# Kernel optimization log

Measured on AMD Instinct MI355X. Metric: run time of the kernel, lower is better.

## Reference

```python
import jax, jax.numpy as jnp
import numpy as np

H, DH = 8, 16  # num_heads, head_dim (out_feats // num_heads)
NP, NA, NS = 100000, 60000, 1000


def _gat_conv(feat_src, feat_dst, n_dst, src, dst, W, al, ar, b):
    # DGL GATConv (eval mode: feat_drop/attn_drop are identity)
    hs = (feat_src @ W).reshape(-1, H, DH)          # [Ns,H,D]
    hd = (feat_dst @ W).reshape(-1, H, DH)          # [Nd,H,D]
    el = (hs * al).sum(-1)                          # [Ns,H]
    er = (hd * ar).sum(-1)                          # [Nd,H]
    e = jax.nn.leaky_relu(el[src] + er[dst], negative_slope=0.2)  # [E,H]
    # segment softmax over edges sharing a destination node
    emax = jax.ops.segment_max(e, dst, num_segments=n_dst)
    emax = jnp.where(jnp.isfinite(emax), emax, 0.0)
    ee = jnp.exp(e - emax[dst])
    denom = jax.ops.segment_sum(ee, dst, num_segments=n_dst)
    alpha = ee / jnp.maximum(denom[dst], 1e-9)      # [E,H]
    m = jax.ops.segment_sum(alpha[:, :, None] * hs[src], dst, num_segments=n_dst)
    return m.reshape(n_dst, H * DH) + b             # [Nd, out_feats]


def setup_inputs() -> dict:
    key = jax.random.key(0)
    ks = jax.random.split(key, 18)
    Epa, Eps = 300000, 150000
    f32 = jnp.float32
    inp = {
        "feat_paper_0": jax.random.normal(ks[0], (NP, 128), f32),
        "feat_author_0": jax.random.normal(ks[1], (NA, 128), f32),
        "feat_subject_0": jax.random.normal(ks[2], (NS, 128), f32),
        "feat_paper_1": jax.random.normal(ks[3], (NP, 128), f32),
        "feat_author_1": jax.random.normal(ks[4], (NA, 128), f32),
        "feat_subject_1": jax.random.normal(ks[5], (NS, 128), f32),
        "pa_src": jax.random.randint(ks[6], (Epa,), 0, NP, jnp.int32),
        "pa_dst": jax.random.randint(ks[7], (Epa,), 0, NA, jnp.int32),
        "ap_src": jax.random.randint(ks[8], (Epa,), 0, NA, jnp.int32),
        "ap_dst": jax.random.randint(ks[9], (Epa,), 0, NP, jnp.int32),
        "ps_src": jax.random.randint(ks[10], (Eps,), 0, NP, jnp.int32),
        "ps_dst": jax.random.randint(ks[11], (Eps,), 0, NS, jnp.int32),
        "sp_src": jax.random.randint(ks[12], (Eps,), 0, NS, jnp.int32),
        "sp_dst": jax.random.randint(ks[13], (Eps,), 0, NP, jnp.int32),
        "Ws": jax.random.normal(ks[14], (4, 128, 128), f32) * 0.08,
        "als": jax.random.normal(ks[15], (4, H, DH), f32) * 0.1,
        "ars": jax.random.normal(ks[16], (4, H, DH), f32) * 0.1,
        "bs": jnp.zeros((4, 128), f32),
    }
    return inp


def reference(feat_paper_0, feat_author_0, feat_subject_0,
              feat_paper_1, feat_author_1, feat_subject_1,
              pa_src, pa_dst, ap_src, ap_dst, ps_src, ps_dst, sp_src, sp_dst,
              Ws, als, ars, bs):
    def one_input(fp, fa, fs):
        # rel 0: paper->author, 1: author->paper, 2: paper->subject, 3: subject->paper
        h_author = _gat_conv(fp, fa, NA, pa_src, pa_dst, Ws[0], als[0], ars[0], bs[0])
        h_paper_ap = _gat_conv(fa, fp, NP, ap_src, ap_dst, Ws[1], als[1], ars[1], bs[1])
        h_subject = _gat_conv(fp, fs, NS, ps_src, ps_dst, Ws[2], als[2], ars[2], bs[2])
        h_paper_sp = _gat_conv(fs, fp, NP, sp_src, sp_dst, Ws[3], als[3], ars[3], bs[3])
        h_paper = (h_paper_ap + h_paper_sp) * 0.5  # HeteroGraphConv aggregate='mean'
        # act = identity; key order for ACM: [paper, author, subject]
        return jnp.concatenate([h_paper, h_author, h_subject], axis=0)

    out0 = one_input(feat_paper_0, feat_author_0, feat_subject_0)
    out1 = one_input(feat_paper_1, feat_author_1, feat_subject_1)
    return jnp.stack([out0, out1], axis=0)  # [2, NP+NA+NS, 128]
```

## Files before the change

kernel.cpp:

```cpp
#include <hip/hip_runtime.h>

#define NHEAD 8
#define NPAPER 100000
#define NAUTHOR 60000
#define NSUBJ 1000
#define NTOT (NPAPER + NAUTHOR + NSUBJ)
#define NDEG 261000

typedef __attribute__((ext_vector_type(8))) short bf16x8;
typedef __attribute__((ext_vector_type(4))) float f32x4;

__device__ __forceinline__ unsigned short f2bf(float x) {
    unsigned int u = __builtin_bit_cast(unsigned int, x);
    u += 0x7fffu + ((u >> 16) & 1u);
    return (unsigned short)(u >> 16);
}
__device__ __forceinline__ float bf2f_lo(unsigned int v) {
    return __builtin_bit_cast(float, v << 16);
}
__device__ __forceinline__ float bf2f_hi(unsigned int v) {
    return __builtin_bit_cast(float, v & 0xffff0000u);
}

__global__ void prep_kernel(const float* __restrict__ Ws, const float* __restrict__ als,
                            const float* __restrict__ ars,
                            unsigned short* __restrict__ Wt,
                            unsigned short* __restrict__ combo) {
    int idx = blockIdx.x * 256 + threadIdx.x;
    if (idx < 65536) {
        int r = idx >> 14, rem = idx & 16383, c = rem >> 7, k = rem & 127;
        Wt[idx] = f2bf(Ws[(r << 14) + k * 128 + c]);
    } else if (idx < 65536 + 8192) {
        int j = idx - 65536;
        int r = j >> 11, rem = j & 2047, n = rem >> 7, k = rem & 127;
        int p = r ^ 1;
        const float *W, *a;
        if (n < 8) {
            W = Ws + (r << 14) + k * 128 + n * 16;
            a = als + r * 128 + n * 16;
        } else {
            int h = n - 8;
            W = Ws + (p << 14) + k * 128 + h * 16;
            a = ars + p * 128 + h * 16;
        }
        float s = 0.f;
#pragma unroll
        for (int d = 0; d < 16; ++d) s += W[d] * a[d];
        combo[j] = f2bf(s);
    }
}

struct CsrPtrs {
    const int* esrc[4];
    const int* edst[4];
    int ebase[5];
    int nbase[4];
};

__global__ void csr_count(CsrPtrs cp, int* __restrict__ deg) {
    int idx = blockIdx.x * 256 + threadIdx.x;
    if (idx >= cp.ebase[4]) return;
    int r = 0;
    while (idx >= cp.ebase[r + 1]) ++r;
    int e = idx - cp.ebase[r];
    atomicAdd(&deg[cp.nbase[r] + cp.edst[r][e]], 1);
}

__global__ void csr_scatter(CsrPtrs cp, int* __restrict__ cursor,
                            int* __restrict__ srcs) {
    int idx = blockIdx.x * 256 + threadIdx.x;
    if (idx >= cp.ebase[4]) return;
    int r = 0;
    while (idx >= cp.ebase[r + 1]) ++r;
    int e = idx - cp.ebase[r];
    int p = atomicAdd(&cursor[cp.nbase[r] + cp.edst[r][e]], 1);
    srcs[p] = cp.esrc[r][e];
}

__global__ __launch_bounds__(256) void scan_bsum(const int* __restrict__ deg,
                                                 int* __restrict__ bsums, int N) {
    int base = blockIdx.x * 1024 + threadIdx.x * 4;
    int s = 0;
#pragma unroll
    for (int j = 0; j < 4; ++j) {
        int i = base + j;
        if (i < N) s += deg[i];
    }
#pragma unroll
    for (int off = 32; off; off >>= 1) s += __shfl_down(s, off);
    __shared__ int wt[4];
    if ((threadIdx.x & 63) == 0) wt[threadIdx.x >> 6] = s;
    __syncthreads();
    if (threadIdx.x == 0) bsums[blockIdx.x] = wt[0] + wt[1] + wt[2] + wt[3];
}

__global__ __launch_bounds__(256) void scan_small_excl(int* __restrict__ data, int n) {
    int t = threadIdx.x;
    int v = (t < n) ? data[t] : 0;
    int inc = v;
#pragma unroll
    for (int off = 1; off < 64; off <<= 1) {
        int u = __shfl_up(inc, off);
        if ((t & 63) >= off) inc += u;
    }
    __shared__ int wt[4];
    if ((t & 63) == 63) wt[t >> 6] = inc;
    __syncthreads();
    int wo = 0;
    for (int w = 0; w < (t >> 6); ++w) wo += wt[w];
    if (t < n) data[t] = wo + inc - v;
}

__global__ __launch_bounds__(256) void scan_final(const int* __restrict__ deg,
                                                  const int* __restrict__ bsums,
                                                  int* __restrict__ row_ptr,
                                                  int* __restrict__ cursor, int N) {
    int t = threadIdx.x;
    int base = blockIdx.x * 1024 + t * 4;
    int d[4];
    int s = 0;
#pragma unroll
    for (int j = 0; j < 4; ++j) {
        int i = base + j;
        d[j] = (i < N) ? deg[i] : 0;
        s += d[j];
    }
    int inc = s;
#pragma unroll
    for (int off = 1; off < 64; off <<= 1) {
        int u = __shfl_up(inc, off);
        if ((t & 63) >= off) inc += u;
    }
    __shared__ int wt[4];
    if ((t & 63) == 63) wt[t >> 6] = inc;
    __syncthreads();
    int start = bsums[blockIdx.x];
    for (int w = 0; w < (t >> 6); ++w) start += wt[w];
    start += inc - s;
#pragma unroll
    for (int j = 0; j < 4; ++j) {
        int i = base + j;
        if (i < N) {
            row_ptr[i] = start;
            cursor[i] = start;
        }
        start += d[j];
    }
    if (base < N && base + 4 >= N) row_ptr[N] = start;
}

struct ProjArgs {
    const float* A[8];
    const unsigned short* Wt[8];
    const unsigned short* cb[8];
    unsigned short* hs[8];
    float* el[8];
    float* er[8];
    int N[8];
    int blk0[9];
};

__global__ __launch_bounds__(256) void project_kernel(ProjArgs args) {
    int bb = blockIdx.x;
    int t = 0;
    while (bb >= args.blk0[t + 1]) ++t;
    const float* A = args.A[t];
    const unsigned short* Wt = args.Wt[t];
    const unsigned short* cb = args.cb[t];
    unsigned short* hs = args.hs[t];
    float* el = args.el[t];
    float* er = args.er[t];
    const int N = args.N[t];
    const int row0 = (bb - args.blk0[t]) * 64;

    __shared__ unsigned short Abf[64 * 128];
    __shared__ unsigned short Wl[144 * 128];
    const int tid = threadIdx.x;

#pragma unroll
    for (int it = 0; it < 4; ++it) {
        int id = it * 256 + tid;
        int r = id >> 4, c8 = id & 15;
        int row = row0 + r;
        if (row >= N) row = N - 1;
        const float4* ap = reinterpret_cast<const float4*>(A + (size_t)row * 128 + c8 * 8);
        float4 v0 = ap[0], v1 = ap[1];
        uint4 pk;
        pk.x = (unsigned)f2bf(v0.x) | ((unsigned)f2bf(v0.y) << 16);
        pk.y = (unsigned)f2bf(v0.z) | ((unsigned)f2bf(v0.w) << 16);
        pk.z = (unsigned)f2bf(v1.x) | ((unsigned)f2bf(v1.y) << 16);
        pk.w = (unsigned)f2bf(v1.z) | ((unsigned)f2bf(v1.w) << 16);
        *reinterpret_cast<uint4*>(&Abf[(r * 16 + (c8 ^ (r & 15))) * 8]) = pk;
    }
#pragma unroll
    for (int it = 0; it < 9; ++it) {
        int id = it * 256 + tid;
        int r = id >> 4, c8 = id & 15;
        const unsigned short* srcp = (r < 128) ? (Wt + r * 128) : (cb + (r - 128) * 128);
        uint4 v = *reinterpret_cast<const uint4*>(srcp + c8 * 8);
        *reinterpret_cast<uint4*>(&Wl[(r * 16 + (c8 ^ (r & 15))) * 8]) = v;
    }
    __syncthreads();

    const int l = tid & 63;
    const int w = tid >> 6;
    const int lrow = l & 15;
    const int lk8 = l >> 4;

    bf16x8 af[4];
    const int arow = w * 16 + lrow;
#pragma unroll
    for (int ks = 0; ks < 4; ++ks) {
        int c8 = ks * 4 + lk8;
        af[ks] = *reinterpret_cast<const bf16x8*>(
            &Abf[(arow * 16 + (c8 ^ (arow & 15))) * 8]);
    }
    __syncthreads();

#pragma unroll
    for (int t9 = 0; t9 < 9; ++t9) {
        f32x4 acc = f32x4{0.f, 0.f, 0.f, 0.f};
#pragma unroll
        for (int ks = 0; ks < 4; ++ks) {
            int wrow = t9 * 16 + lrow;
            int c8 = ks * 4 + lk8;
            bf16x8 bf = *reinterpret_cast<const bf16x8*>(
                &Wl[(wrow * 16 + (c8 ^ (wrow & 15))) * 8]);
            acc = __builtin_amdgcn_mfma_f32_16x16x32_bf16(af[ks], bf, acc, 0, 0, 0);
        }
        if (t9 < 8) {
#pragma unroll
            for (int r = 0; r < 4; ++r) {
                int rl = w * 16 + lk8 * 4 + r;
                int col = t9 * 16 + lrow;
                Abf[(rl * 16 + ((col >> 3) ^ (rl & 15))) * 8 + (col & 7)] = f2bf(acc[r]);
            }
        } else {
#pragma unroll
            for (int r = 0; r < 4; ++r) {
                int row = row0 + w * 16 + lk8 * 4 + r;
                if (row < N) {
                    if (lrow < 8) el[(size_t)row * 8 + lrow] = acc[r];
                    else er[(size_t)row * 8 + (lrow - 8)] = acc[r];
                }
            }
        }
    }
    __syncthreads();

#pragma unroll
    for (int it = 0; it < 4; ++it) {
        int id = it * 256 + tid;
        int r = id >> 4, c8 = id & 15;
        int row = row0 + r;
        if (row < N) {
            uint4 v = *reinterpret_cast<const uint4*>(&Abf[(r * 16 + (c8 ^ (r & 15))) * 8]);
            *reinterpret_cast<uint4*>(hs + (size_t)row * 128 + c8 * 8) = v;
        }
    }
}

__device__ __forceinline__ void acc_list(int p0, int p1, float erd, int l, int h,
                                         const int* __restrict__ srcs,
                                         const float* __restrict__ el,
                                         const unsigned short* __restrict__ hs,
                                         float* A, float& DS) {
    float a4[4][8];
    float dv[4] = {0.f, 0.f, 0.f, 0.f};
#pragma unroll
    for (int u = 0; u < 4; ++u)
#pragma unroll
        for (int j = 0; j < 8; ++j) a4[u][j] = 0.f;
    int p = p0;
    for (; p + 4 <= p1; p += 4) {
        int sx[4];
#pragma unroll
        for (int u = 0; u < 4; ++u) sx[u] = srcs[p + u];
        float ev[4];
        uint4 q[4];
#pragma unroll
        for (int u = 0; u < 4; ++u) {
            ev[u] = el[(size_t)sx[u] * 8 + h] + erd;
            q[u] = *reinterpret_cast<const uint4*>(hs + (size_t)sx[u] * 128 + l * 8);
        }
#pragma unroll
        for (int u = 0; u < 4; ++u) {
            float e = ev[u];
            e = e > 0.f ? e : 0.2f * e;
            float ee = __expf(e);
            dv[u] += ee;
            a4[u][0] += ee * bf2f_lo(q[u].x);
            a4[u][1] += ee * bf2f_hi(q[u].x);
            a4[u][2] += ee * bf2f_lo(q[u].y);
            a4[u][3] += ee * bf2f_hi(q[u].y);
            a4[u][4] += ee * bf2f_lo(q[u].z);
            a4[u][5] += ee * bf2f_hi(q[u].z);
            a4[u][6] += ee * bf2f_lo(q[u].w);
            a4[u][7] += ee * bf2f_hi(q[u].w);
        }
    }
    for (; p < p1; ++p) {
        int s = srcs[p];
        float e = el[(size_t)s * 8 + h] + erd;
        e = e > 0.f ? e : 0.2f * e;
        float ee = __expf(e);
        uint4 q = *reinterpret_cast<const uint4*>(hs + (size_t)s * 128 + l * 8);
        dv[0] += ee;
        a4[0][0] += ee * bf2f_lo(q.x);
        a4[0][1] += ee * bf2f_hi(q.x);
        a4[0][2] += ee * bf2f_lo(q.y);
        a4[0][3] += ee * bf2f_hi(q.y);
        a4[0][4] += ee * bf2f_lo(q.z);
        a4[0][5] += ee * bf2f_hi(q.z);
        a4[0][6] += ee * bf2f_lo(q.w);
        a4[0][7] += ee * bf2f_hi(q.w);
    }
#pragma unroll
    for (int j = 0; j < 8; ++j) A[j] = a4[0][j] + a4[1][j] + a4[2][j] + a4[3][j];
    DS = dv[0] + dv[1] + dv[2] + dv[3];
}

__global__ __launch_bounds__(256) void agg_author(
    const int* __restrict__ rp, const int* __restrict__ srcs,
    const float* __restrict__ el0, const float* __restrict__ el1,
    const float* __restrict__ er0, const float* __restrict__ er1,
    const unsigned short* __restrict__ hs0, const unsigned short* __restrict__ hs1,
    const float* __restrict__ b, float* __restrict__ out0, float* __restrict__ out1) {
    int g = (blockIdx.x * 256 + threadIdx.x) >> 4;
    int l = threadIdx.x & 15;
    if (g >= 2 * NAUTHOR) return;
    int inp = g >= NAUTHOR;
    int dst = inp ? g - NAUTHOR : g;
    const float* el = inp ? el1 : el0;
    const float* er = inp ? er1 : er0;
    const unsigned short* hs = inp ? hs1 : hs0;
    float* out = inp ? out1 : out0;
    int h = l >> 1;
    int p0 = rp[dst], p1 = rp[dst + 1];
    float erd = er[(size_t)dst * 8 + h];
    float A[8], ds;
    acc_list(p0, p1, erd, l, h, srcs, el, hs, A, ds);
    float inv = 1.f / fmaxf(ds, 1e-9f);
    const float4* bp = reinterpret_cast<const float4*>(b + l * 8);
    float4 b0 = bp[0], b1 = bp[1];
    float4 o0 = make_float4(A[0] * inv + b0.x, A[1] * inv + b0.y,
                            A[2] * inv + b0.z, A[3] * inv + b0.w);
    float4 o1 = make_float4(A[4] * inv + b1.x, A[5] * inv + b1.y,
                            A[6] * inv + b1.z, A[7] * inv + b1.w);
    float* op = out + (size_t)dst * 128 + l * 8;
    reinterpret_cast<float4*>(op)[0] = o0;
    reinterpret_cast<float4*>(op)[1] = o1;
}

__global__ __launch_bounds__(256) void agg_paper(
    const int* __restrict__ rp, const int* __restrict__ srcs,
    const float* __restrict__ el1a, const float* __restrict__ el1b,
    const float* __restrict__ er1a, const float* __restrict__ er1b,
    const unsigned short* __restrict__ hs1a, const unsigned short* __restrict__ hs1b,
    const float* __restrict__ el3a, const float* __restrict__ el3b,
    const float* __restrict__ er3a, const float* __restrict__ er3b,
    const unsigned short* __restrict__ hs3a, const unsigned short* __restrict__ hs3b,
    const float* __restrict__ b1, const float* __restrict__ b3,
    float* __restrict__ out0, float* __restrict__ out1) {
    int g = (blockIdx.x * 256 + threadIdx.x) >> 4;
    int l = threadIdx.x & 15;
    if (g >= 2 * NPAPER) return;
    int inp = g >= NPAPER;
    int dst = inp ? g - NPAPER : g;
    const float* el1 = inp ? el1b : el1a;
    const float* er1 = inp ? er1b : er1a;
    const unsigned short* hs1 = inp ? hs1b : hs1a;
    const float* el3 = inp ? el3b : el3a;
    const float* er3 = inp ? er3b : er3a;
    const unsigned short* hs3 = inp ? hs3b : hs3a;
    float* out = inp ? out1 : out0;
    int h = l >> 1;

    float A1[8], A3[8], d1, d3;
    {
        int p0 = rp[60000 + dst], p1 = rp[60000 + dst + 1];
        acc_list(p0, p1, er1[(size_t)dst * 8 + h], l, h, srcs, el1, hs1, A1, d1);
    }
    {
        int p0 = rp[161000 + dst], p1 = rp[161000 + dst + 1];
        acc_list(p0, p1, er3[(size_t)dst * 8 + h], l, h, srcs, el3, hs3, A3, d3);
    }
    float i1 = 1.f / fmaxf(d1, 1e-9f);
    float i3 = 1.f / fmaxf(d3, 1e-9f);
    const float4* bp1 = reinterpret_cast<const float4*>(b1 + l * 8);
    const float4* bp3 = reinterpret_cast<const float4*>(b3 + l * 8);
    float4 b10 = bp1[0], b11 = bp1[1], b30 = bp3[0], b31 = bp3[1];
    float4 o0, o1;
    o0.x = 0.5f * ((A1[0] * i1 + b10.x) + (A3[0] * i3 + b30.x));
    o0.y = 0.5f * ((A1[1] * i1 + b10.y) + (A3[1] * i3 + b30.y));
    o0.z = 0.5f * ((A1[2] * i1 + b10.z) + (A3[2] * i3 + b30.z));
    o0.w = 0.5f * ((A1[3] * i1 + b10.w) + (A3[3] * i3 + b30.w));
    o1.x = 0.5f * ((A1[4] * i1 + b11.x) + (A3[4] * i3 + b31.x));
    o1.y = 0.5f * ((A1[5] * i1 + b11.y) + (A3[5] * i3 + b31.y));
    o1.z = 0.5f * ((A1[6] * i1 + b11.z) + (A3[6] * i3 + b31.z));
    o1.w = 0.5f * ((A1[7] * i1 + b11.w) + (A3[7] * i3 + b31.w));
    float* op = out + (size_t)dst * 128 + l * 8;
    reinterpret_cast<float4*>(op)[0] = o0;
    reinterpret_cast<float4*>(op)[1] = o1;
}

__global__ __launch_bounds__(256) void agg_subject(
    const int* __restrict__ rp, const int* __restrict__ srcs,
    const float* __restrict__ el0, const float* __restrict__ el1,
    const float* __restrict__ er0, const float* __restrict__ er1,
    const unsigned short* __restrict__ hs0, const unsigned short* __restrict__ hs1,
    const float* __restrict__ b, float* __restrict__ out0, float* __restrict__ out1) {
    int blk = blockIdx.x;
    int inp = blk >= NSUBJ;
    int dst = inp ? blk - NSUBJ : blk;
    const float* el = inp ? el1 : el0;
    const float* er = inp ? er1 : er0;
    const unsigned short* hs = inp ? hs1 : hs0;
    float* out = inp ? out1 : out0;
    int gl = threadIdx.x >> 4;
    int l = threadIdx.x & 15;
    int h = l >> 1;
    int p0 = rp[160000 + dst], p1 = rp[160000 + dst + 1];
    float erd = er[(size_t)dst * 8 + h];
    float a[8];
#pragma unroll
    for (int j = 0; j < 8; ++j) a[j] = 0.f;
    float dsum = 0.f;
    for (int p = p0 + gl; p < p1; p += 16) {
        int s = srcs[p];
        float e = el[(size_t)s * 8 + h] + erd;
        e = e > 0.f ? e : 0.2f * e;
        float ee = __expf(e);
        uint4 q = *reinterpret_cast<const uint4*>(hs + (size_t)s * 128 + l * 8);
        dsum += ee;
        a[0] += ee * bf2f_lo(q.x);
        a[1] += ee * bf2f_hi(q.x);
        a[2] += ee * bf2f_lo(q.y);
        a[3] += ee * bf2f_hi(q.y);
        a[4] += ee * bf2f_lo(q.z);
        a[5] += ee * bf2f_hi(q.z);
        a[6] += ee * bf2f_lo(q.w);
        a[7] += ee * bf2f_hi(q.w);
    }
    __shared__ float Am[16][128];
    __shared__ float Dm[16][8];
#pragma unroll
    for (int j = 0; j < 8; ++j) Am[gl][l * 8 + j] = a[j];
    if ((l & 1) == 0) Dm[gl][h] = dsum;
    __syncthreads();
    int c = threadIdx.x;
    if (c < 128) {
        float s = 0.f, dn = 0.f;
        int hh = c >> 4;
#pragma unroll
        for (int g = 0; g < 16; ++g) {
            s += Am[g][c];
            dn += Dm[g][hh];
        }
        out[(size_t)dst * 128 + c] = s / fmaxf(dn, 1e-9f) + b[c];
    }
}

extern "C" void kernel_launch(void* const* d_in, const int* in_sizes, int n_in,
                              void* d_out, int out_size, void* d_ws, size_t ws_size,
                              hipStream_t stream) {
    const float* Ws4 = (const float*)d_in[14];
    const float* als = (const float*)d_in[15];
    const float* ars = (const float*)d_in[16];
    const float* bs = (const float*)d_in[17];
    float* out = (float*)d_out;

    const int Es[4] = {in_sizes[6], in_sizes[8], in_sizes[10], in_sizes[12]};
    const int Nsrcs[4] = {NPAPER, NAUTHOR, NPAPER, NSUBJ};
    const int Ndsts[4] = {NAUTHOR, NPAPER, NSUBJ, NPAPER};
    const int Etot = Es[0] + Es[1] + Es[2] + Es[3];

    char* wsp = (char*)d_ws;
    auto carve = [&](size_t bytes) {
        char* p = wsp;
        wsp += (bytes + 255) & ~(size_t)255;
        return p;
    };
    unsigned short* Wt = (unsigned short*)carve(4 * 16384 * 2);
    unsigned short* combo = (unsigned short*)carve(4 * 2048 * 2);
    unsigned short* hsb[2][4];
    float* elb[2][4];
    float* erb[2][4];
    for (int i = 0; i < 2; ++i)
        for (int r = 0; r < 4; ++r) {
            hsb[i][r] = (unsigned short*)carve((size_t)Nsrcs[r] * 128 * 2);
            elb[i][r] = (float*)carve((size_t)Nsrcs[r] * 8 * 4);
            erb[i][r] = (float*)carve((size_t)Ndsts[r] * 8 * 4);
        }
    int* deg = (int*)carve((size_t)NDEG * 4);
    int* cursor = (int*)carve((size_t)NDEG * 4);
    int* bsums = (int*)carve(1024);
    int* rp = (int*)carve((size_t)(NDEG + 1) * 4);
    int* scsr = (int*)carve((size_t)Etot * 4);

    CsrPtrs cp;
    cp.esrc[0] = (const int*)d_in[6];  cp.edst[0] = (const int*)d_in[7];
    cp.esrc[1] = (const int*)d_in[8];  cp.edst[1] = (const int*)d_in[9];
    cp.esrc[2] = (const int*)d_in[10]; cp.edst[2] = (const int*)d_in[11];
    cp.esrc[3] = (const int*)d_in[12]; cp.edst[3] = (const int*)d_in[13];
    cp.ebase[0] = 0;
    for (int r = 0; r < 4; ++r) cp.ebase[r + 1] = cp.ebase[r] + Es[r];
    cp.nbase[0] = 0;
    cp.nbase[1] = 60000;
    cp.nbase[2] = 160000;
    cp.nbase[3] = 161000;

    prep_kernel<<<288, 256, 0, stream>>>(Ws4, als, ars, Wt, combo);
    hipMemsetAsync(deg, 0, (size_t)NDEG * 4, stream);
    csr_count<<<(Etot + 255) / 256, 256, 0, stream>>>(cp, deg);
    int nb = (NDEG + 1023) / 1024;
    scan_bsum<<<nb, 256, 0, stream>>>(deg, bsums, NDEG);
    scan_small_excl<<<1, 256, 0, stream>>>(bsums, nb);
    scan_final<<<nb, 256, 0, stream>>>(deg, bsums, rp, cursor, NDEG);
    csr_scatter<<<(Etot + 255) / 256, 256, 0, stream>>>(cp, cursor, scsr);

    ProjArgs pa;
    int blk = 0;
    int ti = 0;
    for (int i = 0; i < 2; ++i) {
        const float* feats[3] = {(const float*)d_in[0 + 3 * i],
                                 (const float*)d_in[1 + 3 * i],
                                 (const float*)d_in[2 + 3 * i]};
        const int srcT[4] = {0, 2, 1, 3};
        for (int k = 0; k < 4; ++k) {
            int r = srcT[k];
            const int featT[4] = {0, 1, 0, 2};
            const float* A = feats[featT[r]];
            int N = Nsrcs[r];
            pa.A[ti] = A;
            pa.Wt[ti] = Wt + (size_t)r * 16384;
            pa.cb[ti] = combo + (size_t)r * 2048;
            pa.hs[ti] = hsb[i][r];
            pa.el[ti] = elb[i][r];
            pa.er[ti] = erb[i][r ^ 1];
            pa.N[ti] = N;
            pa.blk0[ti] = blk;
            blk += (N + 63) / 64;
            ++ti;
        }
    }
    pa.blk0[8] = blk;
    project_kernel<<<blk, 256, 0, stream>>>(pa);

    float* out0 = out;
    float* out1 = out + (size_t)NTOT * 128;

    agg_author<<<(2 * NAUTHOR * 16 + 255) / 256, 256, 0, stream>>>(
        rp, scsr, elb[0][0], elb[1][0], erb[0][0], erb[1][0], hsb[0][0], hsb[1][0],
        bs + 0, out0 + (size_t)NPAPER * 128, out1 + (size_t)NPAPER * 128);
    agg_paper<<<(2 * NPAPER * 16 + 255) / 256, 256, 0, stream>>>(
        rp, scsr,
        elb[0][1], elb[1][1], erb[0][1], erb[1][1], hsb[0][1], hsb[1][1],
        elb[0][3], elb[1][3], erb[0][3], erb[1][3], hsb[0][3], hsb[1][3],
        bs + 128, bs + 384, out0, out1);
    agg_subject<<<2 * NSUBJ, 256, 0, stream>>>(
        rp, scsr, elb[0][2], elb[1][2], erb[0][2], erb[1][2], hsb[0][2], hsb[1][2],
        bs + 256, out0 + (size_t)(NPAPER + NAUTHOR) * 128,
        out1 + (size_t)(NPAPER + NAUTHOR) * 128);
}
```

Baseline: 402.8 us.

## Fuse launches: memset into prep, count into projection, single aggregation kernel

```diff
diff --git a/kernel.cpp b/kernel.cpp
--- a/kernel.cpp
+++ b/kernel.cpp
@@ -25,8 +25,14 @@
 __global__ void prep_kernel(const float* __restrict__ Ws, const float* __restrict__ als,
                             const float* __restrict__ ars,
                             unsigned short* __restrict__ Wt,
-                            unsigned short* __restrict__ combo) {
-    int idx = blockIdx.x * 256 + threadIdx.x;
+                            unsigned short* __restrict__ combo, int* __restrict__ deg) {
+    int b = blockIdx.x;
+    if (b >= 288) {
+        int idx = (b - 288) * 1024 + threadIdx.x * 4;
+        if (idx < NDEG) *reinterpret_cast<int4*>(&deg[idx]) = int4{0, 0, 0, 0};
+        return;
+    }
+    int idx = b * 256 + threadIdx.x;
     if (idx < 65536) {
         int r = idx >> 14, rem = idx & 16383, c = rem >> 7, k = rem & 127;
         Wt[idx] = f2bf(Ws[(r << 14) + k * 128 + c]);
@@ -50,132 +56,110 @@
     }
 }
 
-struct CsrPtrs {
-    const int* esrc[4];
+__device__ __forceinline__ void stage_W(unsigned short* Wl, const unsigned short* Wt,
+                                        const unsigned short* cb, int tid) {
+#pragma unroll
+    for (int it = 0; it < 9; ++it) {
+        int id = it * 256 + tid;
+        int r = id >> 4, c8 = id & 15;
+        const unsigned short* srcp = (r < 128) ? (Wt + r * 128) : (cb + (r - 128) * 128);
+        uint4 v = *reinterpret_cast<const uint4*>(srcp + c8 * 8);
+        *reinterpret_cast<uint4*>(&Wl[(r * 16 + (c8 ^ (r & 15))) * 8]) = v;
+    }
+}
+
+__device__ __forceinline__ void mfma_set(const unsigned short* Wl, unsigned short* Abf,
+                                         const bf16x8* af, int tid, int row0, int N,
+                                         float* __restrict__ el, float* __restrict__ er) {
+    const int l = tid & 63, w = tid >> 6, lrow = l & 15, lk8 = l >> 4;
+#pragma unroll
+    for (int t9 = 0; t9 < 9; ++t9) {
+        f32x4 acc = f32x4{0.f, 0.f, 0.f, 0.f};
+#pragma unroll
+        for (int ks = 0; ks < 4; ++ks) {
+            int wrow = t9 * 16 + lrow;
+            int c8 = ks * 4 + lk8;
+            bf16x8 bf = *reinterpret_cast<const bf16x8*>(
+                &Wl[(wrow * 16 + (c8 ^ (wrow & 15))) * 8]);
+            acc = __builtin_amdgcn_mfma_f32_16x16x32_bf16(af[ks], bf, acc, 0, 0, 0);
+        }
+        if (t9 < 8) {
+#pragma unroll
+            for (int r = 0; r < 4; ++r) {
+                int rl = w * 16 + lk8 * 4 + r;
+                int col = t9 * 16 + lrow;
+                Abf[(rl * 16 + ((col >> 3) ^ (rl & 15))) * 8 + (col & 7)] = f2bf(acc[r]);
+            }
+        } else {
+#pragma unroll
+            for (int r = 0; r < 4; ++r) {
+                int row = row0 + w * 16 + lk8 * 4 + r;
+                if (row < N) {
+                    if (lrow < 8) el[(size_t)row * 8 + lrow] = acc[r];
+                    else er[(size_t)row * 8 + (lrow - 8)] = acc[r];
+                }
+            }
+        }
+    }
+}
+
+__device__ __forceinline__ void store_hs(const unsigned short* Abf,
+                                         unsigned short* __restrict__ hs, int tid,
+                                         int row0, int N) {
+#pragma unroll
+    for (int it = 0; it < 4; ++it) {
+        int id = it * 256 + tid;
+        int r = id >> 4, c8 = id & 15;
+        int row = row0 + r;
+        if (row < N) {
+            uint4 v = *reinterpret_cast<const uint4*>(&Abf[(r * 16 + (c8 ^ (r & 15))) * 8]);
+            *reinterpret_cast<uint4*>(hs + (size_t)row * 128 + c8 * 8) = v;
+        }
+    }
+}
+
+struct PCArgs {
     const int* edst[4];
     int ebase[5];
     int nbase[4];
+    int* deg;
+    int cblk;
+    const float* A[6];
+    int N[6];
+    int blk0[7];
+    const unsigned short* Wt1[6];
+    const unsigned short* cb1[6];
+    unsigned short* hs1[6];
+    float* el1[6];
+    float* er1[6];
+    const unsigned short* Wt2[6];
+    const unsigned short* cb2[6];
+    unsigned short* hs2[6];
+    float* el2[6];
+    float* er2[6];
+    int has2[6];
 };
 
-__global__ void csr_count(CsrPtrs cp, int* __restrict__ deg) {
-    int idx = blockIdx.x * 256 + threadIdx.x;
-    if (idx >= cp.ebase[4]) return;
-    int r = 0;
-    while (idx >= cp.ebase[r + 1]) ++r;
-    int e = idx - cp.ebase[r];
-    atomicAdd(&deg[cp.nbase[r] + cp.edst[r][e]], 1);
-}
-
-__global__ void csr_scatter(CsrPtrs cp, int* __restrict__ cursor,
-                            int* __restrict__ srcs) {
-    int idx = blockIdx.x * 256 + threadIdx.x;
-    if (idx >= cp.ebase[4]) return;
-    int r = 0;
-    while (idx >= cp.ebase[r + 1]) ++r;
-    int e = idx - cp.ebase[r];
-    int p = atomicAdd(&cursor[cp.nbase[r] + cp.edst[r][e]], 1);
-    srcs[p] = cp.esrc[r][e];
-}
-
-__global__ __launch_bounds__(256) void scan_bsum(const int* __restrict__ deg,
-                                                 int* __restrict__ bsums, int N) {
-    int base = blockIdx.x * 1024 + threadIdx.x * 4;
-    int s = 0;
-#pragma unroll
-    for (int j = 0; j < 4; ++j) {
-        int i = base + j;
-        if (i < N) s += deg[i];
-    }
-#pragma unroll
-    for (int off = 32; off; off >>= 1) s += __shfl_down(s, off);
-    __shared__ int wt[4];
-    if ((threadIdx.x & 63) == 0) wt[threadIdx.x >> 6] = s;
-    __syncthreads();
-    if (threadIdx.x == 0) bsums[blockIdx.x] = wt[0] + wt[1] + wt[2] + wt[3];
-}
-
-__global__ __launch_bounds__(256) void scan_small_excl(int* __restrict__ data, int n) {
-    int t = threadIdx.x;
-    int v = (t < n) ? data[t] : 0;
-    int inc = v;
-#pragma unroll
-    for (int off = 1; off < 64; off <<= 1) {
-        int u = __shfl_up(inc, off);
-        if ((t & 63) >= off) inc += u;
-    }
-    __shared__ int wt[4];
-    if ((t & 63) == 63) wt[t >> 6] = inc;
-    __syncthreads();
-    int wo = 0;
-    for (int w = 0; w < (t >> 6); ++w) wo += wt[w];
-    if (t < n) data[t] = wo + inc - v;
-}
-
-__global__ __launch_bounds__(256) void scan_final(const int* __restrict__ deg,
-                                                  const int* __restrict__ bsums,
-                                                  int* __restrict__ row_ptr,
-                                                  int* __restrict__ cursor, int N) {
-    int t = threadIdx.x;
-    int base = blockIdx.x * 1024 + t * 4;
-    int d[4];
-    int s = 0;
-#pragma unroll
-    for (int j = 0; j < 4; ++j) {
-        int i = base + j;
-        d[j] = (i < N) ? deg[i] : 0;
-        s += d[j];
-    }
-    int inc = s;
-#pragma unroll
-    for (int off = 1; off < 64; off <<= 1) {
-        int u = __shfl_up(inc, off);
-        if ((t & 63) >= off) inc += u;
-    }
-    __shared__ int wt[4];
-    if ((t & 63) == 63) wt[t >> 6] = inc;
-    __syncthreads();
-    int start = bsums[blockIdx.x];
-    for (int w = 0; w < (t >> 6); ++w) start += wt[w];
-    start += inc - s;
-#pragma unroll
-    for (int j = 0; j < 4; ++j) {
-        int i = base + j;
-        if (i < N) {
-            row_ptr[i] = start;
-            cursor[i] = start;
-        }
-        start += d[j];
-    }
-    if (base < N && base + 4 >= N) row_ptr[N] = start;
-}
-
-struct ProjArgs {
-    const float* A[8];
-    const unsigned short* Wt[8];
-    const unsigned short* cb[8];
-    unsigned short* hs[8];
-    float* el[8];
-    float* er[8];
-    int N[8];
-    int blk0[9];
-};
-
-__global__ __launch_bounds__(256) void project_kernel(ProjArgs args) {
-    int bb = blockIdx.x;
-    int t = 0;
-    while (bb >= args.blk0[t + 1]) ++t;
-    const float* A = args.A[t];
-    const unsigned short* Wt = args.Wt[t];
-    const unsigned short* cb = args.cb[t];
-    unsigned short* hs = args.hs[t];
-    float* el = args.el[t];
-    float* er = args.er[t];
-    const int N = args.N[t];
-    const int row0 = (bb - args.blk0[t]) * 64;
-
+__global__ __launch_bounds__(256) void project_count(PCArgs a) {
     __shared__ unsigned short Abf[64 * 128];
     __shared__ unsigned short Wl[144 * 128];
+    int bb = blockIdx.x;
     const int tid = threadIdx.x;
+    if (bb < a.cblk) {
+        int idx = bb * 256 + tid;
+        if (idx < a.ebase[4]) {
+            int r = 0;
+            while (idx >= a.ebase[r + 1]) ++r;
+            atomicAdd(&a.deg[a.nbase[r] + a.edst[r][idx - a.ebase[r]]], 1);
+        }
+        return;
+    }
+    bb -= a.cblk;
+    int t = 0;
+    while (bb >= a.blk0[t + 1]) ++t;
+    const int row0 = (bb - a.blk0[t]) * 64;
+    const int N = a.N[t];
+    const float* A = a.A[t];
 
 #pragma unroll
     for (int it = 0; it < 4; ++it) {
@@ -192,21 +176,10 @@
         pk.w = (unsigned)f2bf(v1.z) | ((unsigned)f2bf(v1.w) << 16);
         *reinterpret_cast<uint4*>(&Abf[(r * 16 + (c8 ^ (r & 15))) * 8]) = pk;
     }
-#pragma unroll
-    for (int it = 0; it < 9; ++it) {
-        int id = it * 256 + tid;
-        int r = id >> 4, c8 = id & 15;
-        const unsigned short* srcp = (r < 128) ? (Wt + r * 128) : (cb + (r - 128) * 128);
-        uint4 v = *reinterpret_cast<const uint4*>(srcp + c8 * 8);
-        *reinterpret_cast<uint4*>(&Wl[(r * 16 + (c8 ^ (r & 15))) * 8]) = v;
-    }
-    __syncthreads();
-
-    const int l = tid & 63;
-    const int w = tid >> 6;
-    const int lrow = l & 15;
-    const int lk8 = l >> 4;
-
+    stage_W(Wl, a.Wt1[t], a.cb1[t], tid);
+    __syncthreads();
+
+    const int l = tid & 63, w = tid >> 6, lrow = l & 15, lk8 = l >> 4;
     bf16x8 af[4];
     const int arow = w * 16 + lrow;
 #pragma unroll
@@ -217,47 +190,100 @@
     }
     __syncthreads();
 
-#pragma unroll
-    for (int t9 = 0; t9 < 9; ++t9) {
-        f32x4 acc = f32x4{0.f, 0.f, 0.f, 0.f};
-#pragma unroll
-        for (int ks = 0; ks < 4; ++ks) {
-            int wrow = t9 * 16 + lrow;
-            int c8 = ks * 4 + lk8;
-            bf16x8 bf = *reinterpret_cast<const bf16x8*>(
-                &Wl[(wrow * 16 + (c8 ^ (wrow & 15))) * 8]);
-            acc = __builtin_amdgcn_mfma_f32_16x16x32_bf16(af[ks], bf, acc, 0, 0, 0);
-        }
-        if (t9 < 8) {
-#pragma unroll
-            for (int r = 0; r < 4; ++r) {
-                int rl = w * 16 + lk8 * 4 + r;
-                int col = t9 * 16 + lrow;
-                Abf[(rl * 16 + ((col >> 3) ^ (rl & 15))) * 8 + (col & 7)] = f2bf(acc[r]);
-            }
-        } else {
-#pragma unroll
-            for (int r = 0; r < 4; ++r) {
-                int row = row0 + w * 16 + lk8 * 4 + r;
-                if (row < N) {
-                    if (lrow < 8) el[(size_t)row * 8 + lrow] = acc[r];
-                    else er[(size_t)row * 8 + (lrow - 8)] = acc[r];
-                }
-            }
-        }
-    }
-    __syncthreads();
-
-#pragma unroll
-    for (int it = 0; it < 4; ++it) {
-        int id = it * 256 + tid;
-        int r = id >> 4, c8 = id & 15;
-        int row = row0 + r;
-        if (row < N) {
-            uint4 v = *reinterpret_cast<const uint4*>(&Abf[(r * 16 + (c8 ^ (r & 15))) * 8]);
-            *reinterpret_cast<uint4*>(hs + (size_t)row * 128 + c8 * 8) = v;
-        }
-    }
+    mfma_set(Wl, Abf, af, tid, row0, N, a.el1[t], a.er1[t]);
+    __syncthreads();
+    store_hs(Abf, a.hs1[t], tid, row0, N);
+    if (!a.has2[t]) return;
+    stage_W(Wl, a.Wt2[t], a.cb2[t], tid);
+    __syncthreads();
+    mfma_set(Wl, Abf, af, tid, row0, N, a.el2[t], a.er2[t]);
+    __syncthreads();
+    store_hs(Abf, a.hs2[t], tid, row0, N);
+}
+
+__global__ __launch_bounds__(256) void scan_bsum(const int* __restrict__ deg,
+                                                 int* __restrict__ bsums, int N) {
+    int base = blockIdx.x * 1024 + threadIdx.x * 4;
+    int s = 0;
+#pragma unroll
+    for (int j = 0; j < 4; ++j) {
+        int i = base + j;
+        if (i < N) s += deg[i];
+    }
+#pragma unroll
+    for (int off = 32; off; off >>= 1) s += __shfl_down(s, off);
+    __shared__ int wt[4];
+    if ((threadIdx.x & 63) == 0) wt[threadIdx.x >> 6] = s;
+    __syncthreads();
+    if (threadIdx.x == 0) bsums[blockIdx.x] = wt[0] + wt[1] + wt[2] + wt[3];
+}
+
+__global__ __launch_bounds__(256) void scan_final(const int* __restrict__ deg,
+                                                  const int* __restrict__ bsums,
+                                                  int* __restrict__ row_ptr,
+                                                  int* __restrict__ cursor, int N) {
+    int t = threadIdx.x;
+    __shared__ int s_start;
+    __shared__ int wsum[4];
+    {
+        int acc = 0;
+        for (int i = t; i < (int)blockIdx.x; i += 256) acc += bsums[i];
+#pragma unroll
+        for (int off = 32; off; off >>= 1) acc += __shfl_down(acc, off);
+        if ((t & 63) == 0) wsum[t >> 6] = acc;
+        __syncthreads();
+        if (t == 0) s_start = wsum[0] + wsum[1] + wsum[2] + wsum[3];
+        __syncthreads();
+    }
+    int base = blockIdx.x * 1024 + t * 4;
+    int d[4];
+    int s = 0;
+#pragma unroll
+    for (int j = 0; j < 4; ++j) {
+        int i = base + j;
+        d[j] = (i < N) ? deg[i] : 0;
+        s += d[j];
+    }
+    int inc = s;
+#pragma unroll
+    for (int off = 1; off < 64; off <<= 1) {
+        int u = __shfl_up(inc, off);
+        if ((t & 63) >= off) inc += u;
+    }
+    __shared__ int wt[4];
+    if ((t & 63) == 63) wt[t >> 6] = inc;
+    __syncthreads();
+    int start = s_start;
+    for (int w = 0; w < (t >> 6); ++w) start += wt[w];
+    start += inc - s;
+#pragma unroll
+    for (int j = 0; j < 4; ++j) {
+        int i = base + j;
+        if (i < N) {
+            row_ptr[i] = start;
+            cursor[i] = start;
+        }
+        start += d[j];
+    }
+    if (base < N && base + 4 >= N) row_ptr[N] = start;
+}
+
+struct CsrPtrs {
+    const int* esrc[4];
+    const int* edst[4];
+    int ebase[5];
+    int nbase[4];
+};
+
+__global__ void csr_scatter(CsrPtrs cp, int* __restrict__ cursor,
+                            int* __restrict__ srcs) {
+    int idx = blockIdx.x * 256 + threadIdx.x;
+    if (idx >= cp.ebase[4]) return;
+    int r = 0;
+    while (idx >= cp.ebase[r + 1]) ++r;
+    int e = idx - cp.ebase[r];
+    int p = atomicAdd(&cursor[cp.nbase[r] + cp.edst[r][e]], 1);
+    srcs[p] = cp.esrc[r][e];
 }
 
 __device__ __forceinline__ void acc_list(int p0, int p1, float erd, int l, int h,
@@ -320,144 +346,120 @@
     DS = dv[0] + dv[1] + dv[2] + dv[3];
 }
 
-__global__ __launch_bounds__(256) void agg_author(
-    const int* __restrict__ rp, const int* __restrict__ srcs,
-    const float* __restrict__ el0, const float* __restrict__ el1,
-    const float* __restrict__ er0, const float* __restrict__ er1,
-    const unsigned short* __restrict__ hs0, const unsigned short* __restrict__ hs1,
-    const float* __restrict__ b, float* __restrict__ out0, float* __restrict__ out1) {
-    int g = (blockIdx.x * 256 + threadIdx.x) >> 4;
-    int l = threadIdx.x & 15;
-    if (g >= 2 * NAUTHOR) return;
-    int inp = g >= NAUTHOR;
-    int dst = inp ? g - NAUTHOR : g;
-    const float* el = inp ? el1 : el0;
-    const float* er = inp ? er1 : er0;
-    const unsigned short* hs = inp ? hs1 : hs0;
-    float* out = inp ? out1 : out0;
-    int h = l >> 1;
-    int p0 = rp[dst], p1 = rp[dst + 1];
-    float erd = er[(size_t)dst * 8 + h];
-    float A[8], ds;
-    acc_list(p0, p1, erd, l, h, srcs, el, hs, A, ds);
-    float inv = 1.f / fmaxf(ds, 1e-9f);
-    const float4* bp = reinterpret_cast<const float4*>(b + l * 8);
-    float4 b0 = bp[0], b1 = bp[1];
-    float4 o0 = make_float4(A[0] * inv + b0.x, A[1] * inv + b0.y,
-                            A[2] * inv + b0.z, A[3] * inv + b0.w);
-    float4 o1 = make_float4(A[4] * inv + b1.x, A[5] * inv + b1.y,
-                            A[6] * inv + b1.z, A[7] * inv + b1.w);
-    float* op = out + (size_t)dst * 128 + l * 8;
-    reinterpret_cast<float4*>(op)[0] = o0;
-    reinterpret_cast<float4*>(op)[1] = o1;
-}
-
-__global__ __launch_bounds__(256) void agg_paper(
-    const int* __restrict__ rp, const int* __restrict__ srcs,
-    const float* __restrict__ el1a, const float* __restrict__ el1b,
-    const float* __restrict__ er1a, const float* __restrict__ er1b,
-    const unsigned short* __restrict__ hs1a, const unsigned short* __restrict__ hs1b,
-    const float* __restrict__ el3a, const float* __restrict__ el3b,
-    const float* __restrict__ er3a, const float* __restrict__ er3b,
-    const unsigned short* __restrict__ hs3a, const unsigned short* __restrict__ hs3b,
-    const float* __restrict__ b1, const float* __restrict__ b3,
-    float* __restrict__ out0, float* __restrict__ out1) {
-    int g = (blockIdx.x * 256 + threadIdx.x) >> 4;
-    int l = threadIdx.x & 15;
-    if (g >= 2 * NPAPER) return;
-    int inp = g >= NPAPER;
-    int dst = inp ? g - NPAPER : g;
-    const float* el1 = inp ? el1b : el1a;
-    const float* er1 = inp ? er1b : er1a;
-    const unsigned short* hs1 = inp ? hs1b : hs1a;
-    const float* el3 = inp ? el3b : el3a;
-    const float* er3 = inp ? er3b : er3a;
-    const unsigned short* hs3 = inp ? hs3b : hs3a;
-    float* out = inp ? out1 : out0;
-    int h = l >> 1;
-
-    float A1[8], A3[8], d1, d3;
-    {
-        int p0 = rp[60000 + dst], p1 = rp[60000 + dst + 1];
-        acc_list(p0, p1, er1[(size_t)dst * 8 + h], l, h, srcs, el1, hs1, A1, d1);
-    }
-    {
-        int p0 = rp[161000 + dst], p1 = rp[161000 + dst + 1];
-        acc_list(p0, p1, er3[(size_t)dst * 8 + h], l, h, srcs, el3, hs3, A3, d3);
-    }
-    float i1 = 1.f / fmaxf(d1, 1e-9f);
-    float i3 = 1.f / fmaxf(d3, 1e-9f);
-    const float4* bp1 = reinterpret_cast<const float4*>(b1 + l * 8);
-    const float4* bp3 = reinterpret_cast<const float4*>(b3 + l * 8);
-    float4 b10 = bp1[0], b11 = bp1[1], b30 = bp3[0], b31 = bp3[1];
-    float4 o0, o1;
-    o0.x = 0.5f * ((A1[0] * i1 + b10.x) + (A3[0] * i3 + b30.x));
-    o0.y = 0.5f * ((A1[1] * i1 + b10.y) + (A3[1] * i3 + b30.y));
-    o0.z = 0.5f * ((A1[2] * i1 + b10.z) + (A3[2] * i3 + b30.z));
-    o0.w = 0.5f * ((A1[3] * i1 + b10.w) + (A3[3] * i3 + b30.w));
-    o1.x = 0.5f * ((A1[4] * i1 + b11.x) + (A3[4] * i3 + b31.x));
-    o1.y = 0.5f * ((A1[5] * i1 + b11.y) + (A3[5] * i3 + b31.y));
-    o1.z = 0.5f * ((A1[6] * i1 + b11.z) + (A3[6] * i3 + b31.z));
-    o1.w = 0.5f * ((A1[7] * i1 + b11.w) + (A3[7] * i3 + b31.w));
-    float* op = out + (size_t)dst * 128 + l * 8;
-    reinterpret_cast<float4*>(op)[0] = o0;
-    reinterpret_cast<float4*>(op)[1] = o1;
-}
-
-__global__ __launch_bounds__(256) void agg_subject(
-    const int* __restrict__ rp, const int* __restrict__ srcs,
-    const float* __restrict__ el0, const float* __restrict__ el1,
-    const float* __restrict__ er0, const float* __restrict__ er1,
-    const unsigned short* __restrict__ hs0, const unsigned short* __restrict__ hs1,
-    const float* __restrict__ b, float* __restrict__ out0, float* __restrict__ out1) {
+#define PB 12500
+#define AB 7500
+#define SB 2000
+
+struct AggArgs {
+    const int* rp;
+    const int* srcs;
+    const float* el[8];
+    const float* er[8];
+    const unsigned short* hs[8];
+    const float* bs;
+    float* out0;
+    float* out1;
+};
+
+__global__ __launch_bounds__(256) void mega_agg(AggArgs a) {
     int blk = blockIdx.x;
-    int inp = blk >= NSUBJ;
-    int dst = inp ? blk - NSUBJ : blk;
-    const float* el = inp ? el1 : el0;
-    const float* er = inp ? er1 : er0;
-    const unsigned short* hs = inp ? hs1 : hs0;
-    float* out = inp ? out1 : out0;
-    int gl = threadIdx.x >> 4;
-    int l = threadIdx.x & 15;
-    int h = l >> 1;
-    int p0 = rp[160000 + dst], p1 = rp[160000 + dst + 1];
-    float erd = er[(size_t)dst * 8 + h];
-    float a[8];
-#pragma unroll
-    for (int j = 0; j < 8; ++j) a[j] = 0.f;
-    float dsum = 0.f;
-    for (int p = p0 + gl; p < p1; p += 16) {
-        int s = srcs[p];
-        float e = el[(size_t)s * 8 + h] + erd;
-        e = e > 0.f ? e : 0.2f * e;
-        float ee = __expf(e);
-        uint4 q = *reinterpret_cast<const uint4*>(hs + (size_t)s * 128 + l * 8);
-        dsum += ee;
-        a[0] += ee * bf2f_lo(q.x);
-        a[1] += ee * bf2f_hi(q.x);
-        a[2] += ee * bf2f_lo(q.y);
-        a[3] += ee * bf2f_hi(q.y);
-        a[4] += ee * bf2f_lo(q.z);
-        a[5] += ee * bf2f_hi(q.z);
-        a[6] += ee * bf2f_lo(q.w);
-        a[7] += ee * bf2f_hi(q.w);
-    }
     __shared__ float Am[16][128];
     __shared__ float Dm[16][8];
-#pragma unroll
-    for (int j = 0; j < 8; ++j) Am[gl][l * 8 + j] = a[j];
-    if ((l & 1) == 0) Dm[gl][h] = dsum;
-    __syncthreads();
-    int c = threadIdx.x;
-    if (c < 128) {
-        float s = 0.f, dn = 0.f;
-        int hh = c >> 4;
-#pragma unroll
-        for (int g = 0; g < 16; ++g) {
-            s += Am[g][c];
-            dn += Dm[g][hh];
-        }
-        out[(size_t)dst * 128 + c] = s / fmaxf(dn, 1e-9f) + b[c];
+
+    if (blk < PB) {
+        int g = blk * 16 + (threadIdx.x >> 4);
+        int l = threadIdx.x & 15, h = l >> 1;
+        int inp = g >= NPAPER;
+        int dst = inp ? g - NPAPER : g;
+        float* out = (inp ? a.out1 : a.out0) + (size_t)dst * 128 + l * 8;
+        float A1[8], A3[8], d1, d3;
+        acc_list(a.rp[60000 + dst], a.rp[60000 + dst + 1],
+                 a.er[inp * 4 + 1][(size_t)dst * 8 + h], l, h, a.srcs,
+                 a.el[inp * 4 + 1], a.hs[inp * 4 + 1], A1, d1);
+        acc_list(a.rp[161000 + dst], a.rp[161000 + dst + 1],
+                 a.er[inp * 4 + 3][(size_t)dst * 8 + h], l, h, a.srcs,
+                 a.el[inp * 4 + 3], a.hs[inp * 4 + 3], A3, d3);
+        float i1 = 1.f / fmaxf(d1, 1e-9f);
+        float i3 = 1.f / fmaxf(d3, 1e-9f);
+        const float4* bp1 = reinterpret_cast<const float4*>(a.bs + 128 + l * 8);
+        const float4* bp3 = reinterpret_cast<const float4*>(a.bs + 384 + l * 8);
+        float4 b10 = bp1[0], b11 = bp1[1], b30 = bp3[0], b31 = bp3[1];
+        float4 o0, o1;
+        o0.x = 0.5f * ((A1[0] * i1 + b10.x) + (A3[0] * i3 + b30.x));
+        o0.y = 0.5f * ((A1[1] * i1 + b10.y) + (A3[1] * i3 + b30.y));
+        o0.z = 0.5f * ((A1[2] * i1 + b10.z) + (A3[2] * i3 + b30.z));
+        o0.w = 0.5f * ((A1[3] * i1 + b10.w) + (A3[3] * i3 + b30.w));
+        o1.x = 0.5f * ((A1[4] * i1 + b11.x) + (A3[4] * i3 + b31.x));
+        o1.y = 0.5f * ((A1[5] * i1 + b11.y) + (A3[5] * i3 + b31.y));
+        o1.z = 0.5f * ((A1[6] * i1 + b11.z) + (A3[6] * i3 + b31.z));
+        o1.w = 0.5f * ((A1[7] * i1 + b11.w) + (A3[7] * i3 + b31.w));
+        reinterpret_cast<float4*>(out)[0] = o0;
+        reinterpret_cast<float4*>(out)[1] = o1;
+    } else if (blk < PB + AB) {
+        int g = (blk - PB) * 16 + (threadIdx.x >> 4);
+        int l = threadIdx.x & 15, h = l >> 1;
+        int inp = g >= NAUTHOR;
+        int dst = inp ? g - NAUTHOR : g;
+        float* out = (inp ? a.out1 : a.out0) + (size_t)(NPAPER + dst) * 128 + l * 8;
+        float A[8], ds;
+        acc_list(a.rp[dst], a.rp[dst + 1], a.er[inp * 4 + 0][(size_t)dst * 8 + h], l, h,
+                 a.srcs, a.el[inp * 4 + 0], a.hs[inp * 4 + 0], A, ds);
+        float inv = 1.f / fmaxf(ds, 1e-9f);
+        const float4* bp = reinterpret_cast<const float4*>(a.bs + l * 8);
+        float4 b0 = bp[0], b1 = bp[1];
+        float4 o0 = make_float4(A[0] * inv + b0.x, A[1] * inv + b0.y,
+                                A[2] * inv + b0.z, A[3] * inv + b0.w);
+        float4 o1 = make_float4(A[4] * inv + b1.x, A[5] * inv + b1.y,
+                                A[6] * inv + b1.z, A[7] * inv + b1.w);
+        reinterpret_cast<float4*>(out)[0] = o0;
+        reinterpret_cast<float4*>(out)[1] = o1;
+    } else {
+        int b2 = blk - (PB + AB);
+        int inp = b2 >= NSUBJ;
+        int dst = inp ? b2 - NSUBJ : b2;
+        const float* el = a.el[inp * 4 + 2];
+        const float* er = a.er[inp * 4 + 2];
+        const unsigned short* hs = a.hs[inp * 4 + 2];
+        float* out = (inp ? a.out1 : a.out0) + (size_t)(NPAPER + NAUTHOR + dst) * 128;
+        int gl = threadIdx.x >> 4;
+        int l = threadIdx.x & 15, h = l >> 1;
+        int p0 = a.rp[160000 + dst], p1 = a.rp[160000 + dst + 1];
+        float erd = er[(size_t)dst * 8 + h];
+        float acc8[8];
+#pragma unroll
+        for (int j = 0; j < 8; ++j) acc8[j] = 0.f;
+        float dsum = 0.f;
+        for (int p = p0 + gl; p < p1; p += 16) {
+            int s = a.srcs[p];
+            float e = el[(size_t)s * 8 + h] + erd;
+            e = e > 0.f ? e : 0.2f * e;
+            float ee = __expf(e);
+            uint4 q = *reinterpret_cast<const uint4*>(hs + (size_t)s * 128 + l * 8);
+            dsum += ee;
+            acc8[0] += ee * bf2f_lo(q.x);
+            acc8[1] += ee * bf2f_hi(q.x);
+            acc8[2] += ee * bf2f_lo(q.y);
+            acc8[3] += ee * bf2f_hi(q.y);
+            acc8[4] += ee * bf2f_lo(q.z);
+            acc8[5] += ee * bf2f_hi(q.z);
+            acc8[6] += ee * bf2f_lo(q.w);
+            acc8[7] += ee * bf2f_hi(q.w);
+        }
+#pragma unroll
+        for (int j = 0; j < 8; ++j) Am[gl][l * 8 + j] = acc8[j];
+        if ((l & 1) == 0) Dm[gl][h] = dsum;
+        __syncthreads();
+        int c = threadIdx.x;
+        if (c < 128) {
+            float s = 0.f, dn = 0.f;
+            int hh = c >> 4;
+#pragma unroll
+            for (int g = 0; g < 16; ++g) {
+                s += Am[g][c];
+                dn += Dm[g][hh];
+            }
+            out[c] = s / fmaxf(dn, 1e-9f) + a.bs[256 + c];
+        }
     }
 }
 
@@ -498,68 +500,76 @@
     int* rp = (int*)carve((size_t)(NDEG + 1) * 4);
     int* scsr = (int*)carve((size_t)Etot * 4);
 
+    prep_kernel<<<288 + (NDEG + 1023) / 1024, 256, 0, stream>>>(Ws4, als, ars, Wt,
+                                                                combo, deg);
+
+    PCArgs pc;
+    pc.edst[0] = (const int*)d_in[7];
+    pc.edst[1] = (const int*)d_in[9];
+    pc.edst[2] = (const int*)d_in[11];
+    pc.edst[3] = (const int*)d_in[13];
+    pc.ebase[0] = 0;
+    for (int r = 0; r < 4; ++r) pc.ebase[r + 1] = pc.ebase[r] + Es[r];
+    pc.nbase[0] = 0;
+    pc.nbase[1] = 60000;
+    pc.nbase[2] = 160000;
+    pc.nbase[3] = 161000;
+    pc.deg = deg;
+    pc.cblk = (Etot + 255) / 256;
+
+    int blk = 0;
+    for (int ti = 0; ti < 6; ++ti) {
+        int i = ti & 1;
+        int nodeT = ti >> 1;
+        const int relOf[3] = {0, 1, 3};
+        int r = relOf[nodeT];
+        const float* feats[3] = {(const float*)d_in[0 + 3 * i],
+                                 (const float*)d_in[1 + 3 * i],
+                                 (const float*)d_in[2 + 3 * i]};
+        pc.A[ti] = feats[nodeT];
+        pc.N[ti] = (nodeT == 0) ? NPAPER : (nodeT == 1 ? NAUTHOR : NSUBJ);
+        pc.blk0[ti] = blk;
+        blk += (pc.N[ti] + 63) / 64;
+        pc.Wt1[ti] = Wt + (size_t)r * 16384;
+        pc.cb1[ti] = combo + (size_t)r * 2048;
+        pc.hs1[ti] = hsb[i][r];
+        pc.el1[ti] = elb[i][r];
+        pc.er1[ti] = erb[i][r ^ 1];
+        pc.has2[ti] = (nodeT == 0);
+        int r2 = 2;
+        pc.Wt2[ti] = Wt + (size_t)r2 * 16384;
+        pc.cb2[ti] = combo + (size_t)r2 * 2048;
+        pc.hs2[ti] = hsb[i][r2];
+        pc.el2[ti] = elb[i][r2];
+        pc.er2[ti] = erb[i][r2 ^ 1];
+    }
+    pc.blk0[6] = blk;
+    project_count<<<pc.cblk + blk, 256, 0, stream>>>(pc);
+
+    int nb = (NDEG + 1023) / 1024;
+    scan_bsum<<<nb, 256, 0, stream>>>(deg, bsums, NDEG);
+    scan_final<<<nb, 256, 0, stream>>>(deg, bsums, rp, cursor, NDEG);
+
     CsrPtrs cp;
     cp.esrc[0] = (const int*)d_in[6];  cp.edst[0] = (const int*)d_in[7];
     cp.esrc[1] = (const int*)d_in[8];  cp.edst[1] = (const int*)d_in[9];
     cp.esrc[2] = (const int*)d_in[10]; cp.edst[2] = (const int*)d_in[11];
     cp.esrc[3] = (const int*)d_in[12]; cp.edst[3] = (const int*)d_in[13];
-    cp.ebase[0] = 0;
-    for (int r = 0; r < 4; ++r) cp.ebase[r + 1] = cp.ebase[r] + Es[r];
-    cp.nbase[0] = 0;
-    cp.nbase[1] = 60000;
-    cp.nbase[2] = 160000;
-    cp.nbase[3] = 161000;
-
-    prep_kernel<<<288, 256, 0, stream>>>(Ws4, als, ars, Wt, combo);
-    hipMemsetAsync(deg, 0, (size_t)NDEG * 4, stream);
-    csr_count<<<(Etot + 255) / 256, 256, 0, stream>>>(cp, deg);
-    int nb = (NDEG + 1023) / 1024;
-    scan_bsum<<<nb, 256, 0, stream>>>(deg, bsums, NDEG);
-    scan_small_excl<<<1, 256, 0, stream>>>(bsums, nb);
-    scan_final<<<nb, 256, 0, stream>>>(deg, bsums, rp, cursor, NDEG);
+    for (int r = 0; r < 5; ++r) cp.ebase[r] = pc.ebase[r];
+    for (int r = 0; r < 4; ++r) cp.nbase[r] = pc.nbase[r];
     csr_scatter<<<(Etot + 255) / 256, 256, 0, stream>>>(cp, cursor, scsr);
 
-    ProjArgs pa;
-    int blk = 0;
-    int ti = 0;
-    for (int i = 0; i < 2; ++i) {
-        const float* feats[3] = {(const float*)d_in[0 + 3 * i],
-                                 (const float*)d_in[1 + 3 * i],
-                                 (const float*)d_in[2 + 3 * i]};
-        const int srcT[4] = {0, 2, 1, 3};
-        for (int k = 0; k < 4; ++k) {
-            int r = srcT[k];
-            const int featT[4] = {0, 1, 0, 2};
-            const float* A = feats[featT[r]];
-            int N = Nsrcs[r];
-            pa.A[ti] = A;
-            pa.Wt[ti] = Wt + (size_t)r * 16384;
-            pa.cb[ti] = combo + (size_t)r * 2048;
-            pa.hs[ti] = hsb[i][r];
-            pa.el[ti] = elb[i][r];
-            pa.er[ti] = erb[i][r ^ 1];
-            pa.N[ti] = N;
-            pa.blk0[ti] = blk;
-            blk += (N + 63) / 64;
-            ++ti;
-        }
-    }
-    pa.blk0[8] = blk;
-    project_kernel<<<blk, 256, 0, stream>>>(pa);
-
-    float* out0 = out;
-    float* out1 = out + (size_t)NTOT * 128;
-
-    agg_author<<<(2 * NAUTHOR * 16 + 255) / 256, 256, 0, stream>>>(
-        rp, scsr, elb[0][0], elb[1][0], erb[0][0], erb[1][0], hsb[0][0], hsb[1][0],
-        bs + 0, out0 + (size_t)NPAPER * 128, out1 + (size_t)NPAPER * 128);
-    agg_paper<<<(2 * NPAPER * 16 + 255) / 256, 256, 0, stream>>>(
-        rp, scsr,
-        elb[0][1], elb[1][1], erb[0][1], erb[1][1], hsb[0][1], hsb[1][1],
-        elb[0][3], elb[1][3], erb[0][3], erb[1][3], hsb[0][3], hsb[1][3],
-        bs + 128, bs + 384, out0, out1);
-    agg_subject<<<2 * NSUBJ, 256, 0, stream>>>(
-        rp, scsr, elb[0][2], elb[1][2], erb[0][2], erb[1][2], hsb[0][2], hsb[1][2],
-        bs + 256, out0 + (size_t)(NPAPER + NAUTHOR) * 128,
-        out1 + (size_t)(NPAPER + NAUTHOR) * 128);
-}
+    AggArgs ag;
+    ag.rp = rp;
+    ag.srcs = scsr;
+    for (int i = 0; i < 2; ++i)
+        for (int r = 0; r < 4; ++r) {
+            ag.el[i * 4 + r] = elb[i][r];
+            ag.er[i * 4 + r] = erb[i][r];
+            ag.hs[i * 4 + r] = hsb[i][r];
+        }
+    ag.bs = bs;
+    ag.out0 = out;
+    ag.out1 = out + (size_t)NTOT * 128;
+    mega_agg<<<PB + AB + SB, 256, 0, stream>>>(ag);
+}
```

New measurement: 384.0 us. -4.7%, faster.
